# Kernel optimization log

Measured on AMD Instinct MI355X. Metric: run time of the kernel, lower is better.

Reference implementation:

```python
import jax, jax.numpy as jnp
import numpy as np

B, T, D = 16, 1024, 768
H = 12
HD = D // H
MLP = 3072


def _layernorm(x, g, b, eps=1e-5):
    mu = jnp.mean(x, axis=-1, keepdims=True)
    var = jnp.var(x, axis=-1, keepdims=True)
    return (x - mu) * jax.lax.rsqrt(var + eps) * g + b


def setup_inputs() -> dict:
    key = jax.random.key(0)
    ks = jax.random.split(key, 12)
    s_d = 1.0 / np.sqrt(D)
    s_m = 1.0 / np.sqrt(MLP)
    return {
        "x": jax.random.normal(ks[0], (B, T, D), dtype=jnp.float32),
        "Wq": jax.random.uniform(ks[1], (D, D), jnp.float32, -s_d, s_d),
        "bq": jnp.zeros((D,), jnp.float32),
        "Wk": jax.random.uniform(ks[2], (D, D), jnp.float32, -s_d, s_d),
        "bk": jnp.zeros((D,), jnp.float32),
        "Wv": jax.random.uniform(ks[3], (D, D), jnp.float32, -s_d, s_d),
        "bv": jnp.zeros((D,), jnp.float32),
        "Wo": jax.random.uniform(ks[4], (D, D), jnp.float32, -s_d, s_d),
        "bo": jnp.zeros((D,), jnp.float32),
        "ln1_g": jnp.ones((D,), jnp.float32),
        "ln1_b": jnp.zeros((D,), jnp.float32),
        "ln2_g": jnp.ones((D,), jnp.float32),
        "ln2_b": jnp.zeros((D,), jnp.float32),
        "W1": jax.random.uniform(ks[5], (D, MLP), jnp.float32, -s_d, s_d),
        "b1": jnp.zeros((MLP,), jnp.float32),
        "W2": jax.random.uniform(ks[6], (MLP, D), jnp.float32, -s_m, s_m),
        "b2": jnp.zeros((D,), jnp.float32),
    }


def reference(x, Wq, bq, Wk, bk, Wv, bv, Wo, bo, ln1_g, ln1_b, ln2_g, ln2_b, W1, b1, W2, b2):
    h = _layernorm(x, ln1_g, ln1_b)
    # QKV projections -> [B, H, T, HD]
    q = (h @ Wq + bq).reshape(B, T, H, HD).transpose(0, 2, 1, 3)
    k = (h @ Wk + bk).reshape(B, T, H, HD).transpose(0, 2, 1, 3)
    v = (h @ Wv + bv).reshape(B, T, H, HD).transpose(0, 2, 1, 3)
    # NOTE: original divides by sqrt(input_dim), not sqrt(head_dim)
    scores = jnp.einsum('bhtf,bhjf->bhtj', q, k) / jnp.sqrt(jnp.float32(D))
    score = jax.nn.softmax(scores, axis=-1)
    attn = jnp.einsum('bhij,bhjf->bihf', score, v)  # [B, T, H, HD]
    attn_out = attn.reshape(B, T, D) @ Wo + bo
    out = attn_out + x
    h2 = _layernorm(out, ln2_g, ln2_b)
    # MLP: Linear -> GELU -> Linear -> GELU (GELU after 2nd linear is in the source)
    m = jax.nn.gelu(h2 @ W1 + b1, approximate=False)
    m = jax.nn.gelu(m @ W2 + b2, approximate=False)
    return m + out
```

## Files before the change

### kernel.cpp

```cpp
#include <hip/hip_runtime.h>
#include <hip/hip_bf16.h>
#include <math.h>

#define D_MODEL 768
#define T_SEQ   1024
#define B_BATCH 16
#define MLP_DIM 3072
#define M_ROWS  (B_BATCH * T_SEQ)

typedef __attribute__((ext_vector_type(8))) __bf16          bf16x8;
typedef __attribute__((ext_vector_type(4))) __bf16          bf16x4;
typedef __attribute__((ext_vector_type(4))) float           f32x4;

__device__ __forceinline__ float bf2f(unsigned short u) {
  union { unsigned int u; float f; } w; w.u = ((unsigned int)u) << 16; return w.f;
}
__device__ __forceinline__ unsigned short f2bf(float f) {
  union { float f; unsigned int u; } w; w.f = f;
  unsigned int r = (w.u + 0x7fffu + ((w.u >> 16) & 1u)) >> 16;
  return (unsigned short)r;
}
__device__ __forceinline__ float gelu_f(float x) {
  return 0.5f * x * (1.0f + erff(x * 0.70710678118654752f));
}
__device__ __forceinline__ void gload16(const void* g, void* l) {
  __builtin_amdgcn_global_load_lds(
      (const __attribute__((address_space(1))) unsigned int*)g,
      (__attribute__((address_space(3))) unsigned int*)l, 16, 0, 0);
}

__global__ void wtr_k(const float* __restrict__ src,
                      unsigned short* __restrict__ dst, int R, int C) {
  __shared__ float t[32][33];
  const int c0 = blockIdx.x * 32, r0 = blockIdx.y * 32;
  const int tx = threadIdx.x, ty = threadIdx.y;
  #pragma unroll
  for (int j = 0; j < 32; j += 8)
    t[ty + j][tx] = src[(size_t)(r0 + ty + j) * C + (c0 + tx)];
  __syncthreads();
  #pragma unroll
  for (int j = 0; j < 32; j += 8)
    dst[(size_t)(c0 + ty + j) * R + (r0 + tx)] = f2bf(t[tx][ty + j]);
}

__global__ void bcat_k(const float* __restrict__ a, const float* __restrict__ b,
                       const float* __restrict__ c, float* __restrict__ o) {
  const int i = blockIdx.x * 256 + threadIdx.x;
  if (i < 768) { o[i] = a[i]; o[i + 768] = b[i]; o[i + 1536] = c[i]; }
}

template<int SRC_F32>
__global__ __launch_bounds__(256) void ln_k(const void* __restrict__ src,
    const float* __restrict__ g, const float* __restrict__ b,
    unsigned short* __restrict__ out) {
  const int row = blockIdx.x, tid = threadIdx.x;
  const size_t base = (size_t)row * D_MODEL;
  float v[3];
  #pragma unroll
  for (int i = 0; i < 3; ++i) {
    const int c = tid + (i << 8);
    v[i] = SRC_F32 ? ((const float*)src)[base + c]
                   : bf2f(((const unsigned short*)src)[base + c]);
  }
  float s  = v[0] + v[1] + v[2];
  float sq = v[0]*v[0] + v[1]*v[1] + v[2]*v[2];
  #pragma unroll
  for (int m = 32; m; m >>= 1) { s += __shfl_xor(s, m); sq += __shfl_xor(sq, m); }
  __shared__ float ps[4], pq[4];
  if ((tid & 63) == 0) { ps[tid >> 6] = s; pq[tid >> 6] = sq; }
  __syncthreads();
  s  = ps[0] + ps[1] + ps[2] + ps[3];
  sq = pq[0] + pq[1] + pq[2] + pq[3];
  const float mu  = s * (1.0f / 768.0f);
  const float var = sq * (1.0f / 768.0f) - mu * mu;
  const float inv = rsqrtf(var + 1e-5f);
  #pragma unroll
  for (int i = 0; i < 3; ++i) {
    const int c = tid + (i << 8);
    out[base + c] = f2bf((v[i] - mu) * inv * g[c] + b[c]);
  }
}

template<int EP>
__global__ __launch_bounds__(512) void gemm_k(
    const unsigned short* __restrict__ Au, const unsigned short* __restrict__ Btu,
    const float* __restrict__ bias, void* __restrict__ outv,
    const void* __restrict__ residv, void* __restrict__ aux,
    int M, int N, int K, int cgrp) {
  __shared__ __align__(16) __bf16 SMEM[2 * 32768];
  const __bf16* A  = (const __bf16*)Au;
  const __bf16* Bt = (const __bf16*)Btu;
  const int tid = threadIdx.x;
  const int lane = tid & 63, w = tid >> 6;
  const int wr = w >> 2, wc = w & 3;
  const int lr = lane & 15, lg = lane >> 4;
  const int gx = gridDim.x, gy = gridDim.y;
  const int bid = blockIdx.y * gx + blockIdx.x;
  const int xcd = bid & 7, idx = bid >> 3;
  const int rpx = gx >> 3;
  const int gsz = rpx * cgrp;
  const int grp = idx / gsz, rem = idx - grp * gsz;
  const int rb = rem / cgrp, cc2 = rem - rb * cgrp + grp * cgrp;
  const int brow = (xcd * rpx + rb) * 256;
  const int bcol = cc2 * 256;

  f32x4 acc[8][4];
  #pragma unroll
  for (int m = 0; m < 8; ++m)
    #pragma unroll
    for (int n = 0; n < 4; ++n) acc[m][n] = (f32x4){0.f, 0.f, 0.f, 0.f};

  const int rrs = lane >> 2;
  const int ccs = (lane & 3) << 3;
  const int csw = ccs ^ ((rrs >> 3) << 4);
  const __bf16* sA[4]; const __bf16* sB[4]; int dA[4], dB[4];
  #pragma unroll
  for (int g = 0; g < 4; ++g) {
    const int s = g * 8 + w;
    const int rsrc = (s >> 1) * 16 + rrs;
    const int csrc = (s & 1) * 32 + csw;
    sA[g] = A  + (size_t)(brow + rsrc) * K + csrc;
    sB[g] = Bt + (size_t)(bcol + rsrc) * K + csrc;
    dA[g] = s * 512;
    dB[g] = 16384 + s * 512;
  }

#define STAGE_(buf_, k0_) do {                                     \
    _Pragma("unroll")                                              \
    for (int g = 0; g < 4; ++g) {                                  \
      gload16(sA[g] + (k0_), &SMEM[(buf_) * 32768 + dA[g]]);       \
      gload16(sB[g] + (k0_), &SMEM[(buf_) * 32768 + dB[g]]);       \
    }                                                              \
  } while (0)

  const int rbase = lr * 32 + ((lg << 3) ^ (((lr >> 3) & 1) << 4));

  STAGE_(0, 0);
  int cur = 0;
  for (int k0 = 0; k0 < K; k0 += 64, cur ^= 1) {
    if (k0 + 64 < K) {
      STAGE_(cur ^ 1, k0 + 64);
      asm volatile("s_waitcnt vmcnt(8)" ::: "memory");
    } else {
      asm volatile("s_waitcnt vmcnt(0)" ::: "memory");
    }
    __builtin_amdgcn_s_barrier();
    __builtin_amdgcn_sched_barrier(0);
    const int bb = cur * 32768;
    bf16x8 bfr[4][2];
    #pragma unroll
    for (int n = 0; n < 4; ++n)
      #pragma unroll
      for (int kk = 0; kk < 2; ++kk)
        bfr[n][kk] = *(const bf16x8*)(&SMEM[bb + 16384 + ((wc*4 + n)*2 + kk)*512 + rbase]);
    __builtin_amdgcn_s_setprio(1);
    #pragma unroll
    for (int mq = 0; mq < 2; ++mq) {
      bf16x8 af[4][2];
      #pragma unroll
      for (int ml = 0; ml < 4; ++ml)
        #pragma unroll
        for (int kk = 0; kk < 2; ++kk)
          af[ml][kk] = *(const bf16x8*)(&SMEM[bb + ((wr*8 + mq*4 + ml)*2 + kk)*512 + rbase]);
      #pragma unroll
      for (int ml = 0; ml < 4; ++ml)
        #pragma unroll
        for (int n = 0; n < 4; ++n) {
          acc[mq*4+ml][n] = __builtin_amdgcn_mfma_f32_16x16x32_bf16(af[ml][0], bfr[n][0], acc[mq*4+ml][n], 0, 0, 0);
          acc[mq*4+ml][n] = __builtin_amdgcn_mfma_f32_16x16x32_bf16(af[ml][1], bfr[n][1], acc[mq*4+ml][n], 0, 0, 0);
        }
    }
    __builtin_amdgcn_s_setprio(0);
    asm volatile("s_waitcnt lgkmcnt(0)" ::: "memory");
    __builtin_amdgcn_sched_barrier(0);
    __builtin_amdgcn_s_barrier();
    __builtin_amdgcn_sched_barrier(0);
  }
#undef STAGE_

  const int seg = (EP == 5) ? (bcol / 768) : 0;
  unsigned short* qkvp = nullptr;
  if (EP == 5)
    qkvp = (seg == 0) ? (unsigned short*)outv
         : (seg == 1) ? (unsigned short*)residv : (unsigned short*)aux;

  if (EP == 5 && seg == 2) {
    #pragma unroll
    for (int n = 0; n < 4; ++n) {
      const int col = bcol + wc*64 + n*16 + lr;
      const float bv = bias[col];
      const int colLv = col - 1536;
      #pragma unroll
      for (int m = 0; m < 8; ++m) {
        const int row0 = brow + wr*128 + m*16 + lg*4;
        #pragma unroll
        for (int r2 = 0; r2 < 4; ++r2) {
          const int gr = row0 + r2;
          qkvp[(((size_t)(gr >> 10) * D_MODEL + colLv) << 10) + (gr & 1023)] =
              f2bf(acc[m][n][r2] + bv);
        }
      }
    }
  } else {
    float* Ep = (float*)SMEM + w * 1280;
    #pragma unroll
    for (int m = 0; m < 8; ++m) {
      #pragma unroll
      for (int n = 0; n < 4; ++n) {
        const int col = bcol + wc*64 + n*16 + lr;
        const float bv = bias[col];
        f32x4 st;
        #pragma unroll
        for (int r2 = 0; r2 < 4; ++r2) {
          float v = acc[m][n][r2] + bv;
          if (EP == 1 || EP == 3) v = gelu_f(v);
          st[r2] = v;
        }
        *(f32x4*)(Ep + (n*16 + lr) * 20 + lg*4) = st;
      }
      #pragma unroll
      for (int i2 = 0; i2 < 2; ++i2) {
        const int rowL = i2*8 + (lane >> 3);
        const int colL = (lane & 7) * 8;
        const int grow = brow + wr*128 + m*16 + rowL;
        const int gcol = bcol + wc*64 + colL;
        float v[8];
        #pragma unroll
        for (int j = 0; j < 8; ++j) v[j] = Ep[(colL + j) * 20 + rowL];
        const size_t o = (size_t)grow * N + gcol;
        if (EP == 3) {
          const bf16x8 rv = *(const bf16x8*)((const __bf16*)residv + o);
          float* op = (float*)outv + o;
          float4 o0, o1;
          o0.x = v[0] + (float)rv[0]; o0.y = v[1] + (float)rv[1];
          o0.z = v[2] + (float)rv[2]; o0.w = v[3] + (float)rv[3];
          o1.x = v[4] + (float)rv[4]; o1.y = v[5] + (float)rv[5];
          o1.z = v[6] + (float)rv[6]; o1.w = v[7] + (float)rv[7];
          *(float4*)op = o0; *(float4*)(op + 4) = o1;
        } else if (EP == 2) {
          const float* rp = (const float*)residv + o;
          const float4 r0 = *(const float4*)rp, r1 = *(const float4*)(rp + 4);
          bf16x8 ov;
          ov[0] = (__bf16)(v[0] + r0.x); ov[1] = (__bf16)(v[1] + r0.y);
          ov[2] = (__bf16)(v[2] + r0.z); ov[3] = (__bf16)(v[3] + r0.w);
          ov[4] = (__bf16)(v[4] + r1.x); ov[5] = (__bf16)(v[5] + r1.y);
          ov[6] = (__bf16)(v[6] + r1.z); ov[7] = (__bf16)(v[7] + r1.w);
          *(bf16x8*)((__bf16*)outv + o) = ov;
        } else if (EP == 5) {
          bf16x8 ov;
          #pragma unroll
          for (int j = 0; j < 8; ++j) ov[j] = (__bf16)v[j];
          *(bf16x8*)((__bf16*)qkvp + (size_t)grow * 768 + (gcol - seg * 768)) = ov;
        } else {
          bf16x8 ov;
          #pragma unroll
          for (int j = 0; j < 8; ++j) ov[j] = (__bf16)v[j];
          *(bf16x8*)((__bf16*)outv + o) = ov;
        }
      }
    }
  }
}

__global__ __launch_bounds__(512) void attn_k(
    const unsigned short* qu, const unsigned short* __restrict__ ku,
    const unsigned short* __restrict__ vtu, unsigned short* attn) {
  __shared__ __align__(16) __bf16 Kl[64][72];
  __shared__ __align__(16) __bf16 Vl[64][72];
  __shared__ __align__(16) __bf16 Pl[8][16][72];
  const __bf16* qg  = (const __bf16*)qu;
  const __bf16* kg  = (const __bf16*)ku;
  const __bf16* vtg = (const __bf16*)vtu;
  const int bid = blockIdx.x;
  const int xcd = bid & 7, idx = bid >> 3;
  const int bh = xcd * 24 + (idx >> 2);
  const int b = bh / 12, h = bh % 12;
  const int q0 = (idx & 3) * 256;
  const int tid = threadIdx.x, lane = tid & 63, w = tid >> 6;
  const int lr = lane & 15, lg = lane >> 4;
  const float scale = 0.03608439182435161f;

  bf16x8 qa[2][2];
  #pragma unroll
  for (int g = 0; g < 2; ++g) {
    const int qrow = b * T_SEQ + q0 + w * 32 + g * 16 + lr;
    const __bf16* qp = qg + (size_t)qrow * D_MODEL + h * 64 + lg * 8;
    qa[g][0] = *(const bf16x8*)(qp);
    qa[g][1] = *(const bf16x8*)(qp + 32);
  }

  const __bf16* kb = kg  + (size_t)b * T_SEQ * D_MODEL + h * 64;
  const __bf16* vb = vtg + ((size_t)b * D_MODEL + h * 64) * T_SEQ;

  f32x4 o[2][4];
  float m_run[2] = {-1e30f, -1e30f}, l_run[2] = {0.f, 0.f};
  #pragma unroll
  for (int g = 0; g < 2; ++g)
    #pragma unroll
    for (int m = 0; m < 4; ++m) o[g][m] = (f32x4){0.f, 0.f, 0.f, 0.f};

  for (int kv0 = 0; kv0 < T_SEQ; kv0 += 64) {
    __syncthreads();
    {
      const int r = tid >> 3, c = (tid & 7) << 3;
      *(bf16x8*)(&Kl[r][c]) = *(const bf16x8*)(kb + (size_t)(kv0 + r) * D_MODEL + c);
      *(bf16x8*)(&Vl[r][c]) = *(const bf16x8*)(vb + (size_t)r * T_SEQ + kv0 + c);
    }
    __syncthreads();

    #pragma unroll
    for (int g = 0; g < 2; ++g) {
      f32x4 s[4];
      __builtin_amdgcn_s_setprio(1);
      #pragma unroll
      for (int m = 0; m < 4; ++m) {
        s[m] = (f32x4){0.f, 0.f, 0.f, 0.f};
        const bf16x8 kf0 = *(const bf16x8*)(&Kl[m*16 + lr][lg*8]);
        const bf16x8 kf1 = *(const bf16x8*)(&Kl[m*16 + lr][32 + lg*8]);
        s[m] = __builtin_amdgcn_mfma_f32_16x16x32_bf16(kf0, qa[g][0], s[m], 0, 0, 0);
        s[m] = __builtin_amdgcn_mfma_f32_16x16x32_bf16(kf1, qa[g][1], s[m], 0, 0, 0);
      }
      __builtin_amdgcn_s_setprio(0);
      float sv[4][4], tm = -1e30f;
      #pragma unroll
      for (int m = 0; m < 4; ++m)
        #pragma unroll
        for (int r = 0; r < 4; ++r) {
          sv[m][r] = s[m][r] * scale;
          tm = fmaxf(tm, sv[m][r]);
        }
      tm = fmaxf(tm, __shfl_xor(tm, 16));
      tm = fmaxf(tm, __shfl_xor(tm, 32));
      const float mn = fmaxf(m_run[g], tm);
      const float sc = __expf(m_run[g] - mn);
      float ts = 0.f;
      bf16x4 pk[4];
      #pragma unroll
      for (int m = 0; m < 4; ++m)
        #pragma unroll
        for (int r = 0; r < 4; ++r) {
          const float pp = __expf(sv[m][r] - mn);
          ts += pp;
          pk[m][r] = (__bf16)pp;
        }
      ts += __shfl_xor(ts, 16);
      ts += __shfl_xor(ts, 32);
      l_run[g] = l_run[g] * sc + ts;
      m_run[g] = mn;
      #pragma unroll
      for (int m = 0; m < 4; ++m)
        #pragma unroll
        for (int r = 0; r < 4; ++r) o[g][m][r] *= sc;
      #pragma unroll
      for (int m = 0; m < 4; ++m)
        *(bf16x4*)(&Pl[w][lr][16*m + 4*lg]) = pk[m];
      const bf16x8 pf0 = *(const bf16x8*)(&Pl[w][lr][lg*8]);
      const bf16x8 pf1 = *(const bf16x8*)(&Pl[w][lr][32 + lg*8]);
      __builtin_amdgcn_s_setprio(1);
      #pragma unroll
      for (int m = 0; m < 4; ++m) {
        const bf16x8 vf0 = *(const bf16x8*)(&Vl[m*16 + lr][lg*8]);
        const bf16x8 vf1 = *(const bf16x8*)(&Vl[m*16 + lr][32 + lg*8]);
        o[g][m] = __builtin_amdgcn_mfma_f32_16x16x32_bf16(vf0, pf0, o[g][m], 0, 0, 0);
        o[g][m] = __builtin_amdgcn_mfma_f32_16x16x32_bf16(vf1, pf1, o[g][m], 0, 0, 0);
      }
      __builtin_amdgcn_s_setprio(0);
    }
  }

  #pragma unroll
  for (int g = 0; g < 2; ++g) {
    const float inv = 1.0f / l_run[g];
    const int qrow = b * T_SEQ + q0 + w * 32 + g * 16 + lr;
    unsigned short* op = attn + (size_t)qrow * D_MODEL + h * 64;
    #pragma unroll
    for (int m = 0; m < 4; ++m) {
      bf16x4 ov;
      #pragma unroll
      for (int r = 0; r < 4; ++r) ov[r] = (__bf16)(o[g][m][r] * inv);
      *(bf16x4*)(op + 16*m + 4*lg) = ov;
    }
  }
}

extern "C" void kernel_launch(void* const* d_in, const int* in_sizes, int n_in,
                              void* d_out, int out_size, void* d_ws, size_t ws_size,
                              hipStream_t stream) {
  const float* x   = (const float*)d_in[0];
  const float* Wq  = (const float*)d_in[1];
  const float* bq  = (const float*)d_in[2];
  const float* Wk  = (const float*)d_in[3];
  const float* bk  = (const float*)d_in[4];
  const float* Wv  = (const float*)d_in[5];
  const float* bv  = (const float*)d_in[6];
  const float* Wo  = (const float*)d_in[7];
  const float* bo  = (const float*)d_in[8];
  const float* g1  = (const float*)d_in[9];
  const float* bt1 = (const float*)d_in[10];
  const float* g2  = (const float*)d_in[11];
  const float* bt2 = (const float*)d_in[12];
  const float* W1  = (const float*)d_in[13];
  const float* bb1 = (const float*)d_in[14];
  const float* W2  = (const float*)d_in[15];
  const float* bb2 = (const float*)d_in[16];

  const size_t SZ = (size_t)M_ROWS * D_MODEL * 2;
  char* wp = (char*)d_ws;
  unsigned short* wqkvT = (unsigned short*)wp; wp += (size_t)2304 * 768 * 2;
  unsigned short* woT   = (unsigned short*)wp; wp += (size_t)768 * 768 * 2;
  unsigned short* w1T   = (unsigned short*)wp; wp += (size_t)768 * 3072 * 2;
  unsigned short* w2T   = (unsigned short*)wp; wp += (size_t)768 * 3072 * 2;
  float*          bqkv  = (float*)wp;          wp += ((size_t)2304 * 4 + 255) & ~(size_t)255;
  unsigned short* kbuf  = (unsigned short*)wp; wp += SZ;
  unsigned short* vtb   = (unsigned short*)wp;
  unsigned short* res2  = kbuf;
  unsigned short* hid   = vtb;
  const size_t avail = ws_size - (size_t)(wp - (char*)d_ws);
  const int nch = (avail >= (size_t)M_ROWS * MLP_DIM * 2) ? 1
                : (avail >= (size_t)(M_ROWS / 2) * MLP_DIM * 2) ? 2 : 4;

  unsigned short* qd = (unsigned short*)d_out;
  unsigned short* h1 = qd + (size_t)M_ROWS * D_MODEL;
  unsigned short* h2 = h1;

  const dim3 tb(32, 8, 1);
  wtr_k<<<dim3(24, 24), tb, 0, stream>>>(Wq, wqkvT, 768, 768);
  wtr_k<<<dim3(24, 24), tb, 0, stream>>>(Wk, wqkvT + (size_t)768 * 768, 768, 768);
  wtr_k<<<dim3(24, 24), tb, 0, stream>>>(Wv, wqkvT + (size_t)1536 * 768, 768, 768);
  wtr_k<<<dim3(24, 24), tb, 0, stream>>>(Wo, woT, 768, 768);
  wtr_k<<<dim3(96, 24), tb, 0, stream>>>(W1, w1T, 768, 3072);
  wtr_k<<<dim3(24, 96), tb, 0, stream>>>(W2, w2T, 3072, 768);
  bcat_k<<<3, 256, 0, stream>>>(bq, bk, bv, bqkv);

  ln_k<1><<<M_ROWS, 256, 0, stream>>>(x, g1, bt1, h1);

  gemm_k<5><<<dim3(64, 9), 512, 0, stream>>>(h1, wqkvT, bqkv, qd, kbuf, vtb,
                                             M_ROWS, 2304, 768, 9);

  attn_k<<<dim3(768), 512, 0, stream>>>(qd, kbuf, vtb, qd);

  gemm_k<2><<<dim3(64, 3), 512, 0, stream>>>(qd, woT, bo, res2, x, nullptr,
                                             M_ROWS, 768, 768, 3);

  ln_k<0><<<M_ROWS, 256, 0, stream>>>(res2, g2, bt2, h2);

  const int CH = M_ROWS / nch;
  for (int c = 0; c < nch; ++c) {
    const size_t ro = (size_t)c * CH;
    gemm_k<1><<<dim3(CH / 256, 12), 512, 0, stream>>>(h2 + ro * 768, w1T, bb1,
        hid, nullptr, nullptr, CH, 3072, 768, 6);
    gemm_k<3><<<dim3(CH / 256, 3), 512, 0, stream>>>(hid, w2T, bb2,
        (float*)d_out + ro * 768, res2 + ro * 768, nullptr, CH, 768, 3072, 3);
  }
}
```

Before: 508.3 us.

## Shrink GEMM K-step to 32, prefetch attention K/V tiles, use exp2 softmax

The GEMM main loop now stages 32-wide K slices instead of 64, which halves shared memory to 64KB and changes the LDS swizzle. All A/B fragments are loaded before the MFMA block instead of being interleaved with it. The attention kernel register-prefetches the next K/V tile during the current iteration and folds log2(e) into the score scale so it can use exp2f. Risks include more barriers per K step in the GEMM and less overlap between LDS reads and MFMA, traded against the chance of higher occupancy.

```diff
diff --git a/kernel.cpp b/kernel.cpp
--- a/kernel.cpp
+++ b/kernel.cpp
@@ -87,14 +87,14 @@
     const float* __restrict__ bias, void* __restrict__ outv,
     const void* __restrict__ residv, void* __restrict__ aux,
     int M, int N, int K, int cgrp) {
-  __shared__ __align__(16) __bf16 SMEM[2 * 32768];
+  __shared__ __align__(16) __bf16 SMEM[2 * 16384];
   const __bf16* A  = (const __bf16*)Au;
   const __bf16* Bt = (const __bf16*)Btu;
   const int tid = threadIdx.x;
   const int lane = tid & 63, w = tid >> 6;
   const int wr = w >> 2, wc = w & 3;
   const int lr = lane & 15, lg = lane >> 4;
-  const int gx = gridDim.x, gy = gridDim.y;
+  const int gx = gridDim.x;
   const int bid = blockIdx.y * gx + blockIdx.x;
   const int xcd = bid & 7, idx = bid >> 3;
   const int rpx = gx >> 3;
@@ -112,69 +112,57 @@
 
   const int rrs = lane >> 2;
   const int ccs = (lane & 3) << 3;
-  const int csw = ccs ^ ((rrs >> 3) << 4);
-  const __bf16* sA[4]; const __bf16* sB[4]; int dA[4], dB[4];
-  #pragma unroll
-  for (int g = 0; g < 4; ++g) {
-    const int s = g * 8 + w;
-    const int rsrc = (s >> 1) * 16 + rrs;
-    const int csrc = (s & 1) * 32 + csw;
-    sA[g] = A  + (size_t)(brow + rsrc) * K + csrc;
-    sB[g] = Bt + (size_t)(bcol + rsrc) * K + csrc;
+  const int csw = ccs ^ ((((lane >> 3) & 3)) << 3);
+  const __bf16* sA[2]; const __bf16* sB[2]; int dA[2], dB[2];
+  #pragma unroll
+  for (int g = 0; g < 2; ++g) {
+    const int s = 2 * w + g;
+    sA[g] = A  + (size_t)(brow + s * 16 + rrs) * K + csw;
+    sB[g] = Bt + (size_t)(bcol + s * 16 + rrs) * K + csw;
     dA[g] = s * 512;
-    dB[g] = 16384 + s * 512;
-  }
-
-#define STAGE_(buf_, k0_) do {                                     \
-    _Pragma("unroll")                                              \
-    for (int g = 0; g < 4; ++g) {                                  \
-      gload16(sA[g] + (k0_), &SMEM[(buf_) * 32768 + dA[g]]);       \
-      gload16(sB[g] + (k0_), &SMEM[(buf_) * 32768 + dB[g]]);       \
-    }                                                              \
+    dB[g] = 8192 + s * 512;
+  }
+
+#define STAGE_(nbb_, k0_) do {                              \
+    _Pragma("unroll")                                       \
+    for (int g = 0; g < 2; ++g) {                           \
+      gload16(sA[g] + (k0_), &SMEM[(nbb_) + dA[g]]);        \
+      gload16(sB[g] + (k0_), &SMEM[(nbb_) + dB[g]]);        \
+    }                                                       \
   } while (0)
 
-  const int rbase = lr * 32 + ((lg << 3) ^ (((lr >> 3) & 1) << 4));
+  const int rbase = lr * 32 + ((lg << 3) ^ (((lr >> 1) & 3) << 3));
 
   STAGE_(0, 0);
   int cur = 0;
-  for (int k0 = 0; k0 < K; k0 += 64, cur ^= 1) {
-    if (k0 + 64 < K) {
-      STAGE_(cur ^ 1, k0 + 64);
-      asm volatile("s_waitcnt vmcnt(8)" ::: "memory");
+  for (int k0 = 0; k0 < K; k0 += 32, cur ^= 1) {
+    const int bb  = cur * 16384;
+    const int nbb = (cur ^ 1) * 16384;
+    if (k0 + 32 < K) {
+      STAGE_(nbb, k0 + 32);
+      asm volatile("s_waitcnt vmcnt(4)" ::: "memory");
     } else {
       asm volatile("s_waitcnt vmcnt(0)" ::: "memory");
     }
     __builtin_amdgcn_s_barrier();
     __builtin_amdgcn_sched_barrier(0);
-    const int bb = cur * 32768;
-    bf16x8 bfr[4][2];
+    bf16x8 af[8], bfr[4];
+    #pragma unroll
+    for (int m = 0; m < 8; ++m)
+      af[m] = *(const bf16x8*)(&SMEM[bb + (wr*8 + m)*512 + rbase]);
     #pragma unroll
     for (int n = 0; n < 4; ++n)
-      #pragma unroll
-      for (int kk = 0; kk < 2; ++kk)
-        bfr[n][kk] = *(const bf16x8*)(&SMEM[bb + 16384 + ((wc*4 + n)*2 + kk)*512 + rbase]);
-    __builtin_amdgcn_s_setprio(1);
-    #pragma unroll
-    for (int mq = 0; mq < 2; ++mq) {
-      bf16x8 af[4][2];
-      #pragma unroll
-      for (int ml = 0; ml < 4; ++ml)
-        #pragma unroll
-        for (int kk = 0; kk < 2; ++kk)
-          af[ml][kk] = *(const bf16x8*)(&SMEM[bb + ((wr*8 + mq*4 + ml)*2 + kk)*512 + rbase]);
-      #pragma unroll
-      for (int ml = 0; ml < 4; ++ml)
-        #pragma unroll
-        for (int n = 0; n < 4; ++n) {
-          acc[mq*4+ml][n] = __builtin_amdgcn_mfma_f32_16x16x32_bf16(af[ml][0], bfr[n][0], acc[mq*4+ml][n], 0, 0, 0);
-          acc[mq*4+ml][n] = __builtin_amdgcn_mfma_f32_16x16x32_bf16(af[ml][1], bfr[n][1], acc[mq*4+ml][n], 0, 0, 0);
-        }
-    }
-    __builtin_amdgcn_s_setprio(0);
+      bfr[n] = *(const bf16x8*)(&SMEM[bb + 8192 + (wc*4 + n)*512 + rbase]);
     asm volatile("s_waitcnt lgkmcnt(0)" ::: "memory");
     __builtin_amdgcn_sched_barrier(0);
+    __builtin_amdgcn_s_setprio(1);
+    #pragma unroll
+    for (int m = 0; m < 8; ++m)
+      #pragma unroll
+      for (int n = 0; n < 4; ++n)
+        acc[m][n] = __builtin_amdgcn_mfma_f32_16x16x32_bf16(af[m], bfr[n], acc[m][n], 0, 0, 0);
+    __builtin_amdgcn_s_setprio(0);
     __builtin_amdgcn_s_barrier();
-    __builtin_amdgcn_sched_barrier(0);
   }
 #undef STAGE_
 
@@ -278,7 +266,7 @@
   const int q0 = (idx & 3) * 256;
   const int tid = threadIdx.x, lane = tid & 63, w = tid >> 6;
   const int lr = lane & 15, lg = lane >> 4;
-  const float scale = 0.03608439182435161f;
+  const float scale2 = 0.05206087723865265f;
 
   bf16x8 qa[2][2];
   #pragma unroll
@@ -299,12 +287,17 @@
     #pragma unroll
     for (int m = 0; m < 4; ++m) o[g][m] = (f32x4){0.f, 0.f, 0.f, 0.f};
 
+  const int sr = tid >> 3, sc = (tid & 7) << 3;
+  bf16x8 kr = *(const bf16x8*)(kb + (size_t)sr * D_MODEL + sc);
+  bf16x8 vr = *(const bf16x8*)(vb + (size_t)sr * T_SEQ + sc);
+
   for (int kv0 = 0; kv0 < T_SEQ; kv0 += 64) {
     __syncthreads();
-    {
-      const int r = tid >> 3, c = (tid & 7) << 3;
-      *(bf16x8*)(&Kl[r][c]) = *(const bf16x8*)(kb + (size_t)(kv0 + r) * D_MODEL + c);
-      *(bf16x8*)(&Vl[r][c]) = *(const bf16x8*)(vb + (size_t)r * T_SEQ + kv0 + c);
+    *(bf16x8*)(&Kl[sr][sc]) = kr;
+    *(bf16x8*)(&Vl[sr][sc]) = vr;
+    if (kv0 + 64 < T_SEQ) {
+      kr = *(const bf16x8*)(kb + (size_t)(kv0 + 64 + sr) * D_MODEL + sc);
+      vr = *(const bf16x8*)(vb + (size_t)sr * T_SEQ + kv0 + 64 + sc);
     }
     __syncthreads();
 
@@ -326,31 +319,31 @@
       for (int m = 0; m < 4; ++m)
         #pragma unroll
         for (int r = 0; r < 4; ++r) {
-          sv[m][r] = s[m][r] * scale;
+          sv[m][r] = s[m][r] * scale2;
           tm = fmaxf(tm, sv[m][r]);
         }
       tm = fmaxf(tm, __shfl_xor(tm, 16));
       tm = fmaxf(tm, __shfl_xor(tm, 32));
       const float mn = fmaxf(m_run[g], tm);
-      const float sc = __expf(m_run[g] - mn);
+      const float sc2 = exp2f(m_run[g] - mn);
       float ts = 0.f;
       bf16x4 pk[4];
       #pragma unroll
       for (int m = 0; m < 4; ++m)
         #pragma unroll
         for (int r = 0; r < 4; ++r) {
-          const float pp = __expf(sv[m][r] - mn);
+          const float pp = exp2f(sv[m][r] - mn);
           ts += pp;
           pk[m][r] = (__bf16)pp;
         }
       ts += __shfl_xor(ts, 16);
       ts += __shfl_xor(ts, 32);
-      l_run[g] = l_run[g] * sc + ts;
+      l_run[g] = l_run[g] * sc2 + ts;
       m_run[g] = mn;
       #pragma unroll
       for (int m = 0; m < 4; ++m)
         #pragma unroll
-        for (int r = 0; r < 4; ++r) o[g][m][r] *= sc;
+        for (int r = 0; r < 4; ++r) o[g][m][r] *= sc2;
       #pragma unroll
       for (int m = 0; m < 4; ++m)
         *(bf16x4*)(&Pl[w][lr][16*m + 4*lg]) = pk[m];
```

Result: slower. 544.7 us (+7.2%).
